# Kernel tuning notes

Hardware: AMD Instinct MI355X
Metric: run time of the kernel (lower is better)

## Reference

```python
import jax, jax.numpy as jnp
import numpy as np

B, D, N, F = 1000, 512, 100000, 50  # queries, embed dim (2*rank), entities, filter width
NEG = -1e6


def setup_inputs() -> dict:
    key = jax.random.key(0)
    k1, k2, k3, k4 = jax.random.split(key, 4)
    q = jax.random.normal(k1, (B, D), dtype=jnp.float32)
    rhs = jax.random.normal(k2, (D, N), dtype=jnp.float32)
    filter_idx = jax.random.randint(k3, (B, F), 0, N, dtype=jnp.int64)
    target = jax.random.randint(k4, (B,), 0, N, dtype=jnp.int64)
    return {"q": q, "rhs": rhs, "filter_idx": filter_idx, "target": target}


def reference(q, rhs, filter_idx, target):
    # scores = q @ rhs : [B, N] dense scoring matmul
    scores = q @ rhs
    # targets = self.score(these_queries): dot of query with true entity column -> [B, 1]
    tgt_emb = rhs[:, target]                      # [D, B]
    targets = jnp.sum(q * tgt_emb.T, axis=1, keepdims=True)  # [B, 1]
    # filter masking: filter_out += [true rhs]; scores[i, filter_out] = -1e6
    all_filter = jnp.concatenate([filter_idx, target[:, None]], axis=1)  # [B, F+1]
    rows = jnp.arange(B)[:, None]
    scores = scores.at[rows, all_filter].set(NEG)
    # ranks = 1 + sum(scores >= targets)
    ranks = 1.0 + jnp.sum((scores >= targets).astype(jnp.float32), axis=1)
    return ranks
```

## Files before the change

kernel.cpp:

```cpp
#include <hip/hip_runtime.h>
#include <hip/hip_bf16.h>
#include <cstdint>

#define B_SZ 1000
#define D_SZ 512
#define N_SZ 100000
#define F_SZ 50
#define NEGV -1000000.0f

#define BMr 128
#define BNc 256
#define NT_N3 391
#define NT_B3 8
#define G3 (NT_B3 * NT_N3)
#define CAP3 96

#define T_OFF 0
#define CNT_OFF 4096
#define ENT_OFF 32768
#define QB_OFF  0x200000
#define RT_OFF  0x400000
#define RT_ROWS 100096

typedef __bf16 bf16x8 __attribute__((ext_vector_type(8)));
typedef float f32x4 __attribute__((ext_vector_type(4)));

__device__ __forceinline__ void gl_lds16(const void* g, void* l){
  __builtin_amdgcn_global_load_lds(
      (const __attribute__((address_space(1))) unsigned int*)g,
      (__attribute__((address_space(3))) unsigned int*)l, 16, 0, 0);
}

__global__ void zero_ws(int* p){ p[blockIdx.x * 256 + threadIdx.x] = 0; }

__global__ void cvtq_kernel(const float* __restrict__ q, __bf16* __restrict__ qb){
  int g = blockIdx.x * 256 + threadIdx.x;
  int row = g >> 6;
  int k0 = (g & 63) * 8;
  float4 v0 = make_float4(0.f,0.f,0.f,0.f), v1 = v0;
  if(row < B_SZ){
    v0 = *(const float4*)(q + (size_t)row * D_SZ + k0);
    v1 = *(const float4*)(q + (size_t)row * D_SZ + k0 + 4);
  }
  bf16x8 w = { (__bf16)v0.x,(__bf16)v0.y,(__bf16)v0.z,(__bf16)v0.w,
               (__bf16)v1.x,(__bf16)v1.y,(__bf16)v1.z,(__bf16)v1.w };
  int mt = row >> 7, r = row & 127;
  int kt = k0 >> 5, kq = (k0 >> 3) & 3;
  *(bf16x8*)(qb + ((size_t)(mt*16 + kt)*4 + kq) * 1024 + (size_t)r * 8) = w;
}

__global__ __launch_bounds__(256)
void tconv_kernel(const float* __restrict__ rhs, __bf16* __restrict__ rhsT){
  __shared__ float tile[64][65];
  const int tn = blockIdx.x;
  const int tk = blockIdx.y;
  const int tid = threadIdx.x;
  const int n0 = tn * 64, k0 = tk * 64;
  {
    const int nc = (tid & 15) * 4;
    const int kr0 = tid >> 4;
    #pragma unroll
    for(int i = 0; i < 4; i++){
      int kr = kr0 + i * 16;
      int n = n0 + nc;
      float4 v = (n < N_SZ) ? *(const float4*)(rhs + (size_t)(k0 + kr) * N_SZ + n)
                            : make_float4(0.f,0.f,0.f,0.f);
      tile[kr][nc+0] = v.x; tile[kr][nc+1] = v.y;
      tile[kr][nc+2] = v.z; tile[kr][nc+3] = v.w;
    }
  }
  __syncthreads();
  {
    const int nl = tid & 63;
    const int kc = (tid >> 6) * 16;
    float a[16];
    #pragma unroll
    for(int j = 0; j < 16; j++) a[j] = tile[kc + j][nl];
    bf16x8 w0, w1;
    #pragma unroll
    for(int j = 0; j < 8; j++){ w0[j] = (__bf16)a[j]; w1[j] = (__bf16)a[8 + j]; }
    const int ng = n0 + nl;
    const int nt = ng >> 8, r = ng & 255;
    const int kg = k0 + kc;
    const int kt = kg >> 5, kq0 = (kg >> 3) & 3;
    __bf16* dst = rhsT + ((size_t)(nt*16 + kt)*4 + kq0) * 2048 + (size_t)r * 8;
    *(bf16x8*)dst = w0;
    *(bf16x8*)(dst + 2048) = w1;
  }
}

__global__ void t_kernel(const float* __restrict__ q, const float* __restrict__ rhs,
                         const int* __restrict__ target, float* __restrict__ t){
  int b = blockIdx.x;
  int tid = threadIdx.x;
  int tj = target[b];
  const float* qb = q + (size_t)b * D_SZ;
  float p = qb[tid] * rhs[(size_t)tid * N_SZ + tj]
          + qb[tid + 256] * rhs[(size_t)(tid + 256) * N_SZ + tj];
  for(int off = 32; off; off >>= 1) p += __shfl_down(p, off);
  __shared__ float red[4];
  if((tid & 63) == 0) red[tid >> 6] = p;
  __syncthreads();
  if(tid == 0) t[b] = red[0] + red[1] + red[2] + red[3];
}

__global__ __launch_bounds__(64)
void prep_kernel(const int* __restrict__ filt, const int* __restrict__ target,
                 const float* __restrict__ t, int* __restrict__ cnt,
                 unsigned* __restrict__ entries, float* __restrict__ out){
  const int b = blockIdx.x;
  const int lane = threadIdx.x;
  int v = 0x7fffffff;
  if(lane < F_SZ) v = filt[b * F_SZ + lane];
  else if(lane == F_SZ) v = target[b];
  const bool active = lane <= F_SZ;
  bool first = active;
  #pragma unroll 1
  for(int k = 0; k < F_SZ; k++){
    int o = __shfl(v, k);
    if(active && k < lane && o == v) first = false;
  }
  if(first){
    int bid = (b >> 7) * NT_N3 + (v >> 8);
    int pos = atomicAdd(&cnt[bid], 1);
    if(pos < CAP3)
      entries[(size_t)bid * CAP3 + pos] = (unsigned)(((b & 127) << 8) | (v & 255));
  }
  int nuniq = (int)__popcll(__ballot(first));
  if(lane == 0){
    float tb = t[b];
    out[b] = 1.0f + ((NEGV >= tb) ? (float)nuniq : 0.0f);
  }
}

__global__ __launch_bounds__(512, 4)
void main_kernel(const __bf16* __restrict__ rhsT, const __bf16* __restrict__ qb,
                 const float* __restrict__ t, const int* __restrict__ cnt,
                 const unsigned* __restrict__ entries, float* __restrict__ out){
  __shared__ __attribute__((aligned(16))) __bf16 A2[2][4096];
  __shared__ __attribute__((aligned(16))) __bf16 B2[2][8192];
  __shared__ float tl[128];
  __shared__ unsigned lent[CAP3];
  __shared__ unsigned bm[1024];
  __shared__ int rowc[128];
  __shared__ int lcnt_s;

  const int h = blockIdx.x;
  const int wg = (h & 7) * 391 + (h >> 3);
  const int tile_n = wg >> 3;
  const int tile_b = wg & 7;
  const int bid = tile_b * NT_N3 + tile_n;
  const int tid = threadIdx.x;
  const int n0 = tile_n * BNc;
  const int b0 = tile_b * BMr;

  if(tid < 128){ int b = b0 + tid; tl[tid] = (b < B_SZ) ? t[b] : 0.f; rowc[tid] = 0; }
  if(tid < CAP3) lent[tid] = entries[(size_t)bid * CAP3 + tid];
  if(tid == 0){ int c = cnt[bid]; lcnt_s = (c > CAP3) ? CAP3 : c; }
  if(tid < 512){ bm[tid & 1023] = 0; if(tid < 512) bm[(tid + 512) & 1023] = 0; }

  const int wave = tid >> 6, lane = tid & 63;
  const int quad = lane >> 4, l15 = lane & 15;
  const int wm = wave >> 2, wn = wave & 3;

  const int idxA = quad * 1024 + (wm * 64 + l15) * 8;
  const int idxB = quad * 2048 + (wn * 64 + l15) * 8;

  const __bf16* pAg = qb   + (size_t)tile_b * 65536  + (size_t)tid * 8;
  const __bf16* pBg = rhsT + (size_t)tile_n * 131072 + (size_t)tid * 8;

  f32x4 acc[4][4];
  #pragma unroll
  for(int i = 0; i < 4; i++)
    #pragma unroll
    for(int j = 0; j < 4; j++)
      acc[i][j] = (f32x4){0.f, 0.f, 0.f, 0.f};

  __syncthreads();
  {
    int lc = lcnt_s;
    if(tid < lc){
      unsigned en = lent[tid];
      unsigned row = en >> 8, col = en & 255;
      atomicOr(&bm[row * 8 + (col >> 5)], 1u << (col & 31));
    }
  }
  gl_lds16(pAg,        &A2[0][tid * 8]);
  gl_lds16(pBg,        &B2[0][tid * 8]);
  gl_lds16(pBg + 4096, &B2[0][4096 + tid * 8]);
  pAg += 4096; pBg += 8192;
  asm volatile("s_waitcnt vmcnt(0)" ::: "memory");
  __builtin_amdgcn_s_barrier();
  asm volatile("" ::: "memory");

  #pragma unroll 1
  for(int kt = 0; kt < 16; kt++){
    const int cur = kt & 1, nxt = cur ^ 1;
    if(kt < 15){
      gl_lds16(pAg,        &A2[nxt][tid * 8]);
      gl_lds16(pBg,        &B2[nxt][tid * 8]);
      gl_lds16(pBg + 4096, &B2[nxt][4096 + tid * 8]);
      pAg += 4096; pBg += 8192;
      asm volatile("s_waitcnt vmcnt(3)" ::: "memory");
    } else {
      asm volatile("s_waitcnt vmcnt(0)" ::: "memory");
    }
    __builtin_amdgcn_s_barrier();
    asm volatile("" ::: "memory");

    bf16x8 a4[4], b4[4];
    #pragma unroll
    for(int i = 0; i < 4; i++) a4[i] = *(const bf16x8*)&A2[cur][idxA + i * 128];
    #pragma unroll
    for(int j = 0; j < 4; j++) b4[j] = *(const bf16x8*)&B2[cur][idxB + j * 128];
    __builtin_amdgcn_s_setprio(1);
    #pragma unroll
    for(int i = 0; i < 4; i++)
      #pragma unroll
      for(int j = 0; j < 4; j++)
        acc[i][j] = __builtin_amdgcn_mfma_f32_16x16x32_bf16(a4[i], b4[j], acc[i][j], 0, 0, 0);
    __builtin_amdgcn_s_setprio(0);

    asm volatile("s_waitcnt lgkmcnt(0)" ::: "memory");
    __builtin_amdgcn_s_barrier();
    asm volatile("" ::: "memory");
  }

  #pragma unroll
  for(int i = 0; i < 4; i++){
    #pragma unroll
    for(int r = 0; r < 4; r++){
      const int row = wm*64 + i*16 + quad*4 + r;
      const float trow = tl[row];
      const unsigned w01 = bm[row * 8 + wn * 2];
      const unsigned w23 = bm[row * 8 + wn * 2 + 1];
      int c = 0;
      bool ge[4];
      #pragma unroll
      for(int j = 0; j < 4; j++){
        int ncol = n0 + wn*64 + j*16 + l15;
        ge[j] = (ncol < N_SZ) && (acc[i][j][r] >= trow);
        c += ge[j] ? 1 : 0;
      }
      if(w01 | w23){
        #pragma unroll
        for(int j = 0; j < 4; j++){
          unsigned w = (j < 2) ? w01 : w23;
          if(((w >> ((j & 1) * 16 + l15)) & 1u) && ge[j]) c--;
        }
      }
      c += __shfl_xor(c, 1);
      c += __shfl_xor(c, 2);
      c += __shfl_xor(c, 4);
      c += __shfl_xor(c, 8);
      if(l15 == 0) atomicAdd(&rowc[row], c);
    }
  }
  __syncthreads();
  if(tid < 128){
    int bg = b0 + tid, c = rowc[tid];
    if(bg < B_SZ && c) atomicAdd(&out[bg], (float)c);
  }
}

__global__ __launch_bounds__(256)
void fallback_kernel(const float* __restrict__ q, const float* __restrict__ rhs,
                     const int* __restrict__ filt, const int* __restrict__ target,
                     const float* __restrict__ t, float* __restrict__ out){
  const int b = blockIdx.x;
  const int tid = threadIdx.x;
  __shared__ float qs[D_SZ];
  __shared__ int fs[F_SZ + 1];
  __shared__ float tbs;
  qs[tid] = q[(size_t)b * D_SZ + tid];
  qs[tid + 256] = q[(size_t)b * D_SZ + tid + 256];
  if(tid < F_SZ) fs[tid] = filt[b * F_SZ + tid];
  if(tid == F_SZ) fs[tid] = target[b];
  if(tid == 0) tbs = t[b];
  __syncthreads();
  const float tb = tbs;
  int c = 0;
  const int nend = (blockIdx.y + 1) * 2048 < N_SZ ? (blockIdx.y + 1) * 2048 : N_SZ;
  for(int n = blockIdx.y * 2048 + tid; n < nend; n += 256){
    float s = 0.f;
    for(int k = 0; k < D_SZ; k++) s += qs[k] * rhs[(size_t)k * N_SZ + n];
    if(s >= tb){
      bool m = false;
      for(int i = 0; i <= F_SZ; i++) if(fs[i] == n){ m = true; break; }
      if(!m) c++;
    }
  }
  for(int off = 32; off; off >>= 1) c += __shfl_down(c, off);
  __shared__ int red[4];
  if((tid & 63) == 0) red[tid >> 6] = c;
  __syncthreads();
  if(tid == 0){
    int s = red[0] + red[1] + red[2] + red[3];
    if(s) atomicAdd(&out[b], (float)s);
  }
}

extern "C" void kernel_launch(void* const* d_in, const int* in_sizes, int n_in,
                              void* d_out, int out_size, void* d_ws, size_t ws_size,
                              hipStream_t stream){
  const float* q    = (const float*)d_in[0];
  const float* rhs  = (const float*)d_in[1];
  const int* filt   = (const int*)d_in[2];
  const int* target = (const int*)d_in[3];
  float* out = (float*)d_out;
  char* ws = (char*)d_ws;
  float* t          = (float*)(ws + T_OFF);
  int* cnt          = (int*)(ws + CNT_OFF);
  unsigned* entries = (unsigned*)(ws + ENT_OFF);
  __bf16* qb        = (__bf16*)(ws + QB_OFF);
  __bf16* rhsT      = (__bf16*)(ws + RT_OFF);

  const size_t need = (size_t)RT_OFF + (size_t)RT_ROWS * D_SZ * 2;
  const bool big = ws_size >= need;

  zero_ws<<<32, 256, 0, stream>>>((int*)ws);
  t_kernel<<<B_SZ, 256, 0, stream>>>(q, rhs, target, t);
  prep_kernel<<<B_SZ, 64, 0, stream>>>(filt, target, t, cnt, entries, out);
  if(big){
    cvtq_kernel<<<256, 256, 0, stream>>>(q, qb);
    tconv_kernel<<<dim3(RT_ROWS / 64, 8), 256, 0, stream>>>(rhs, rhsT);
    main_kernel<<<G3, 512, 0, stream>>>(rhsT, qb, t, cnt, entries, out);
  } else {
    fallback_kernel<<<dim3(B_SZ, 49), 256, 0, stream>>>(q, rhs, filt, target, t, out);
  }
}
```

Baseline: 453.6 us.

## Fuse setup kernels and scan per-row filter lists in main kernel

Merges the target-score, filter dedup and query bf16 conversion kernels into one setup kernel, which also drops the workspace zeroing launch. Filters are no longer bucketed per tile with atomics. Each row now stores a 64-entry deduplicated filter list, and every main-kernel block scans all 128×64 entries of its row tile to build its mask bitmap. This cuts launch count and global atomics, but each main block does 16 extra coalesced loads and compares, and the bucket capacity limit goes away.

```diff
diff --git a/kernel.cpp b/kernel.cpp
--- a/kernel.cpp
+++ b/kernel.cpp
@@ -13,14 +13,13 @@
 #define NT_N3 391
 #define NT_B3 8
 #define G3 (NT_B3 * NT_N3)
-#define CAP3 96
 
 #define T_OFF 0
-#define CNT_OFF 4096
-#define ENT_OFF 32768
+#define FENT_OFF 4096
 #define QB_OFF  0x200000
 #define RT_OFF  0x400000
 #define RT_ROWS 100096
+#define SENT 0xFFFFFFFFu
 
 typedef __bf16 bf16x8 __attribute__((ext_vector_type(8)));
 typedef float f32x4 __attribute__((ext_vector_type(4)));
@@ -31,22 +30,57 @@
       (__attribute__((address_space(3))) unsigned int*)l, 16, 0, 0);
 }
 
-__global__ void zero_ws(int* p){ p[blockIdx.x * 256 + threadIdx.x] = 0; }
-
-__global__ void cvtq_kernel(const float* __restrict__ q, __bf16* __restrict__ qb){
-  int g = blockIdx.x * 256 + threadIdx.x;
-  int row = g >> 6;
-  int k0 = (g & 63) * 8;
-  float4 v0 = make_float4(0.f,0.f,0.f,0.f), v1 = v0;
-  if(row < B_SZ){
-    v0 = *(const float4*)(q + (size_t)row * D_SZ + k0);
-    v1 = *(const float4*)(q + (size_t)row * D_SZ + k0 + 4);
-  }
-  bf16x8 w = { (__bf16)v0.x,(__bf16)v0.y,(__bf16)v0.z,(__bf16)v0.w,
-               (__bf16)v1.x,(__bf16)v1.y,(__bf16)v1.z,(__bf16)v1.w };
-  int mt = row >> 7, r = row & 127;
-  int kt = k0 >> 5, kq = (k0 >> 3) & 3;
-  *(bf16x8*)(qb + ((size_t)(mt*16 + kt)*4 + kq) * 1024 + (size_t)r * 8) = w;
+__global__ __launch_bounds__(256)
+void setup_kernel(const float* __restrict__ q, const float* __restrict__ rhs,
+                  const int* __restrict__ filt, const int* __restrict__ target,
+                  float* __restrict__ t, unsigned* __restrict__ fent,
+                  __bf16* __restrict__ qb, float* __restrict__ out){
+  const int b = blockIdx.x;
+  const int tid = threadIdx.x;
+  __shared__ float red[4];
+  __shared__ float tbs;
+  const int tj = target[b];
+  const float* qrow = q + (size_t)b * D_SZ;
+  float p = qrow[tid] * rhs[(size_t)tid * N_SZ + tj]
+          + qrow[tid + 256] * rhs[(size_t)(tid + 256) * N_SZ + tj];
+  for(int off = 32; off; off >>= 1) p += __shfl_down(p, off);
+  if((tid & 63) == 0) red[tid >> 6] = p;
+  __syncthreads();
+  if(tid == 0){ float tb = red[0] + red[1] + red[2] + red[3]; t[b] = tb; tbs = tb; }
+  __syncthreads();
+
+  if(tid < 64){
+    const int lane = tid;
+    int v = 0x7fffffff;
+    if(lane < F_SZ) v = filt[b * F_SZ + lane];
+    else if(lane == F_SZ) v = tj;
+    const bool active = lane <= F_SZ;
+    bool first = active;
+    #pragma unroll 1
+    for(int k = 0; k < F_SZ; k++){
+      int o = __shfl(v, k);
+      if(active && k < lane && o == v) first = false;
+    }
+    fent[(size_t)b * 64 + lane] = first ? (unsigned)v : SENT;
+    int nuniq = (int)__popcll(__ballot(first));
+    if(lane == 0) out[b] = 1.0f + ((NEGV >= tbs) ? (float)nuniq : 0.0f);
+  } else if(tid < 128){
+    const int c = tid - 64;
+    float4 v0 = *(const float4*)(qrow + c * 8);
+    float4 v1 = *(const float4*)(qrow + c * 8 + 4);
+    bf16x8 w = { (__bf16)v0.x,(__bf16)v0.y,(__bf16)v0.z,(__bf16)v0.w,
+                 (__bf16)v1.x,(__bf16)v1.y,(__bf16)v1.z,(__bf16)v1.w };
+    const int mt = b >> 7, r = b & 127, kt = c >> 2, kq = c & 3;
+    *(bf16x8*)(qb + ((size_t)(mt*16 + kt)*4 + kq) * 1024 + (size_t)r * 8) = w;
+  } else if(b == 0){
+    const bf16x8 z = { (__bf16)0.f,(__bf16)0.f,(__bf16)0.f,(__bf16)0.f,
+                       (__bf16)0.f,(__bf16)0.f,(__bf16)0.f,(__bf16)0.f };
+    for(int i = tid - 128; i < 1536; i += 128){
+      int row = 1000 + (i >> 6), c = i & 63;
+      int mt = row >> 7, r = row & 127, kt = c >> 2, kq = c & 3;
+      *(bf16x8*)(qb + ((size_t)(mt*16 + kt)*4 + kq) * 1024 + (size_t)r * 8) = z;
+    }
+  }
 }
 
 __global__ __launch_bounds__(256)
@@ -89,75 +123,26 @@
   }
 }
 
-__global__ void t_kernel(const float* __restrict__ q, const float* __restrict__ rhs,
-                         const int* __restrict__ target, float* __restrict__ t){
-  int b = blockIdx.x;
-  int tid = threadIdx.x;
-  int tj = target[b];
-  const float* qb = q + (size_t)b * D_SZ;
-  float p = qb[tid] * rhs[(size_t)tid * N_SZ + tj]
-          + qb[tid + 256] * rhs[(size_t)(tid + 256) * N_SZ + tj];
-  for(int off = 32; off; off >>= 1) p += __shfl_down(p, off);
-  __shared__ float red[4];
-  if((tid & 63) == 0) red[tid >> 6] = p;
-  __syncthreads();
-  if(tid == 0) t[b] = red[0] + red[1] + red[2] + red[3];
-}
-
-__global__ __launch_bounds__(64)
-void prep_kernel(const int* __restrict__ filt, const int* __restrict__ target,
-                 const float* __restrict__ t, int* __restrict__ cnt,
-                 unsigned* __restrict__ entries, float* __restrict__ out){
-  const int b = blockIdx.x;
-  const int lane = threadIdx.x;
-  int v = 0x7fffffff;
-  if(lane < F_SZ) v = filt[b * F_SZ + lane];
-  else if(lane == F_SZ) v = target[b];
-  const bool active = lane <= F_SZ;
-  bool first = active;
-  #pragma unroll 1
-  for(int k = 0; k < F_SZ; k++){
-    int o = __shfl(v, k);
-    if(active && k < lane && o == v) first = false;
-  }
-  if(first){
-    int bid = (b >> 7) * NT_N3 + (v >> 8);
-    int pos = atomicAdd(&cnt[bid], 1);
-    if(pos < CAP3)
-      entries[(size_t)bid * CAP3 + pos] = (unsigned)(((b & 127) << 8) | (v & 255));
-  }
-  int nuniq = (int)__popcll(__ballot(first));
-  if(lane == 0){
-    float tb = t[b];
-    out[b] = 1.0f + ((NEGV >= tb) ? (float)nuniq : 0.0f);
-  }
-}
-
 __global__ __launch_bounds__(512, 4)
 void main_kernel(const __bf16* __restrict__ rhsT, const __bf16* __restrict__ qb,
-                 const float* __restrict__ t, const int* __restrict__ cnt,
-                 const unsigned* __restrict__ entries, float* __restrict__ out){
+                 const float* __restrict__ t, const unsigned* __restrict__ fent,
+                 float* __restrict__ out){
   __shared__ __attribute__((aligned(16))) __bf16 A2[2][4096];
   __shared__ __attribute__((aligned(16))) __bf16 B2[2][8192];
   __shared__ float tl[128];
-  __shared__ unsigned lent[CAP3];
   __shared__ unsigned bm[1024];
   __shared__ int rowc[128];
-  __shared__ int lcnt_s;
 
   const int h = blockIdx.x;
   const int wg = (h & 7) * 391 + (h >> 3);
   const int tile_n = wg >> 3;
   const int tile_b = wg & 7;
-  const int bid = tile_b * NT_N3 + tile_n;
   const int tid = threadIdx.x;
   const int n0 = tile_n * BNc;
   const int b0 = tile_b * BMr;
 
   if(tid < 128){ int b = b0 + tid; tl[tid] = (b < B_SZ) ? t[b] : 0.f; rowc[tid] = 0; }
-  if(tid < CAP3) lent[tid] = entries[(size_t)bid * CAP3 + tid];
-  if(tid == 0){ int c = cnt[bid]; lcnt_s = (c > CAP3) ? CAP3 : c; }
-  if(tid < 512){ bm[tid & 1023] = 0; if(tid < 512) bm[(tid + 512) & 1023] = 0; }
+  if(tid < 512){ bm[tid] = 0; bm[tid + 512] = 0; }
 
   const int wave = tid >> 6, lane = tid & 63;
   const int quad = lane >> 4, l15 = lane & 15;
@@ -178,11 +163,15 @@
 
   __syncthreads();
   {
-    int lc = lcnt_s;
-    if(tid < lc){
-      unsigned en = lent[tid];
-      unsigned row = en >> 8, col = en & 255;
-      atomicOr(&bm[row * 8 + (col >> 5)], 1u << (col & 31));
+    const unsigned* fb = fent + (size_t)b0 * 64;
+    #pragma unroll
+    for(int e = 0; e < 16; e++){
+      unsigned v = fb[e * 512 + tid];
+      unsigned d = v - (unsigned)n0;
+      if(d < 256u){
+        int bl = (e * 512 + tid) >> 6;
+        atomicOr(&bm[bl * 8 + (d >> 5)], 1u << (d & 31));
+      }
     }
   }
   gl_lds16(pAg,        &A2[0][tid * 8]);
@@ -263,6 +252,43 @@
   }
 }
 
+__global__ void t_kernel(const float* __restrict__ q, const float* __restrict__ rhs,
+                         const int* __restrict__ target, float* __restrict__ t){
+  int b = blockIdx.x;
+  int tid = threadIdx.x;
+  int tj = target[b];
+  const float* qb = q + (size_t)b * D_SZ;
+  float p = qb[tid] * rhs[(size_t)tid * N_SZ + tj]
+          + qb[tid + 256] * rhs[(size_t)(tid + 256) * N_SZ + tj];
+  for(int off = 32; off; off >>= 1) p += __shfl_down(p, off);
+  __shared__ float red[4];
+  if((tid & 63) == 0) red[tid >> 6] = p;
+  __syncthreads();
+  if(tid == 0) t[b] = red[0] + red[1] + red[2] + red[3];
+}
+
+__global__ __launch_bounds__(64)
+void prep_lite(const int* __restrict__ filt, const int* __restrict__ target,
+               const float* __restrict__ t, float* __restrict__ out){
+  const int b = blockIdx.x;
+  const int lane = threadIdx.x;
+  int v = 0x7fffffff;
+  if(lane < F_SZ) v = filt[b * F_SZ + lane];
+  else if(lane == F_SZ) v = target[b];
+  const bool active = lane <= F_SZ;
+  bool first = active;
+  #pragma unroll 1
+  for(int k = 0; k < F_SZ; k++){
+    int o = __shfl(v, k);
+    if(active && k < lane && o == v) first = false;
+  }
+  int nuniq = (int)__popcll(__ballot(first));
+  if(lane == 0){
+    float tb = t[b];
+    out[b] = 1.0f + ((NEGV >= tb) ? (float)nuniq : 0.0f);
+  }
+}
+
 __global__ __launch_bounds__(256)
 void fallback_kernel(const float* __restrict__ q, const float* __restrict__ rhs,
                      const int* __restrict__ filt, const int* __restrict__ target,
@@ -310,22 +336,20 @@
   float* out = (float*)d_out;
   char* ws = (char*)d_ws;
   float* t          = (float*)(ws + T_OFF);
-  int* cnt          = (int*)(ws + CNT_OFF);
-  unsigned* entries = (unsigned*)(ws + ENT_OFF);
+  unsigned* fent    = (unsigned*)(ws + FENT_OFF);
   __bf16* qb        = (__bf16*)(ws + QB_OFF);
   __bf16* rhsT      = (__bf16*)(ws + RT_OFF);
 
   const size_t need = (size_t)RT_OFF + (size_t)RT_ROWS * D_SZ * 2;
   const bool big = ws_size >= need;
 
-  zero_ws<<<32, 256, 0, stream>>>((int*)ws);
-  t_kernel<<<B_SZ, 256, 0, stream>>>(q, rhs, target, t);
-  prep_kernel<<<B_SZ, 64, 0, stream>>>(filt, target, t, cnt, entries, out);
   if(big){
-    cvtq_kernel<<<256, 256, 0, stream>>>(q, qb);
+    setup_kernel<<<B_SZ, 256, 0, stream>>>(q, rhs, filt, target, t, fent, qb, out);
     tconv_kernel<<<dim3(RT_ROWS / 64, 8), 256, 0, stream>>>(rhs, rhsT);
-    main_kernel<<<G3, 512, 0, stream>>>(rhsT, qb, t, cnt, entries, out);
+    main_kernel<<<G3, 512, 0, stream>>>(rhsT, qb, t, fent, out);
   } else {
+    t_kernel<<<B_SZ, 256, 0, stream>>>(q, rhs, target, t);
+    prep_lite<<<B_SZ, 64, 0, stream>>>(filt, target, t, out);
     fallback_kernel<<<dim3(B_SZ, 49), 256, 0, stream>>>(q, rhs, filt, target, t, out);
   }
 }
```

After: 459.9 us. Within noise of the previous version (+1.4%).
